# Performance work log

Measured on AMD Instinct MI355X. Metric: run time of the kernel, lower is better.

The kernel has to match this reference:

```python
import jax, jax.numpy as jnp
import numpy as np

N_NODES = 100000
N_EDGES = 1600000
D_IN = 64
D_HID = 64
D_OUT = 64
TOPK = 32


def _num_params(din, dout):
    return din * dout + dout


def setup_inputs() -> dict:
    key = jax.random.key(0)
    ks = jax.random.split(key, 16)
    x = jax.random.normal(ks[0], (N_NODES, D_IN), dtype=jnp.float32)
    edge_index = jax.random.randint(ks[1], (2, N_EDGES), 0, N_NODES, dtype=jnp.int64)
    # GCN layer params (PyG GCNConv: lin.weight [out,in], bias [out])
    w0 = jax.random.normal(ks[2], (D_HID, D_IN), dtype=jnp.float32) * (1.0 / np.sqrt(D_IN))
    b0 = jnp.zeros((D_HID,), dtype=jnp.float32)
    w1 = jax.random.normal(ks[3], (D_OUT, D_HID), dtype=jnp.float32) * (1.0 / np.sqrt(D_HID))
    b1 = jnp.zeros((D_OUT,), dtype=jnp.float32)
    # summarization vectors p (torch.randn init)
    p0 = jax.random.normal(ks[4], (D_IN,), dtype=jnp.float32)
    p1 = jax.random.normal(ks[5], (D_HID,), dtype=jnp.float32)
    # GRU cells: hidden = num_params, input = topk * feature_dim
    np0 = _num_params(D_IN, D_HID)
    np1 = _num_params(D_HID, D_OUT)
    gi0 = TOPK * D_IN
    gi1 = TOPK * D_HID
    s0 = 1.0 / np.sqrt(np0)
    s1 = 1.0 / np.sqrt(np1)
    wih0 = jax.random.uniform(ks[6], (3 * np0, gi0), jnp.float32, -s0, s0)
    whh0 = jax.random.uniform(ks[7], (3 * np0, np0), jnp.float32, -s0, s0)
    bih0 = jax.random.uniform(ks[8], (3 * np0,), jnp.float32, -s0, s0)
    bhh0 = jax.random.uniform(ks[9], (3 * np0,), jnp.float32, -s0, s0)
    wih1 = jax.random.uniform(ks[10], (3 * np1, gi1), jnp.float32, -s1, s1)
    whh1 = jax.random.uniform(ks[11], (3 * np1, np1), jnp.float32, -s1, s1)
    bih1 = jax.random.uniform(ks[12], (3 * np1,), jnp.float32, -s1, s1)
    bhh1 = jax.random.uniform(ks[13], (3 * np1,), jnp.float32, -s1, s1)
    return {"x": x, "edge_index": edge_index,
            "p0": p0, "p1": p1,
            "w0": w0, "b0": b0, "w1": w1, "b1": b1,
            "wih0": wih0, "whh0": whh0, "bih0": bih0, "bhh0": bhh0,
            "wih1": wih1, "whh1": whh1, "bih1": bih1, "bhh1": bhh1}


def _summarize(h, p, k):
    # attention summary: top-k nodes by h @ p_norm, weighted by tanh(score)
    p_norm = p / (jnp.linalg.norm(p) + 1e-8)
    y = h @ p_norm                      # [N]
    _, idx = jax.lax.top_k(y, k)        # k <= N here, matches torch.topk branch
    w = jnp.tanh(y)
    return h[idx] * w[idx][:, None]     # [k, feat]


def _gru_cell(xv, hv, wih, whh, bih, bhh):
    gi = xv @ wih.T + bih
    gh = hv @ whh.T + bhh
    ir, iz, inew = jnp.split(gi, 3)
    hr, hz, hnew = jnp.split(gh, 3)
    r = jax.nn.sigmoid(ir + hr)
    z = jax.nn.sigmoid(iz + hz)
    n = jnp.tanh(inew + r * hnew)
    return (1.0 - z) * n + z * hv


def _gcn_conv(h, src, dst, weight, bias, n_nodes):
    # PyG GCNConv: x' = x @ W.T; add self-loops; sym-norm aggregation; + bias
    xw = h @ weight.T
    loop = jnp.arange(n_nodes, dtype=src.dtype)
    s = jnp.concatenate([src, loop])
    d = jnp.concatenate([dst, loop])
    deg = jax.ops.segment_sum(jnp.ones(s.shape[0], dtype=xw.dtype), d,
                              num_segments=n_nodes)
    dinv = jnp.where(deg > 0, jax.lax.rsqrt(jnp.maximum(deg, 1e-12)), 0.0)
    norm = dinv[s] * dinv[d]
    msgs = xw[s] * norm[:, None]
    out = jax.ops.segment_sum(msgs, d, num_segments=n_nodes)
    return out + bias


def reference(x, edge_index, p0, p1, w0, b0, w1, b1,
              wih0, whh0, bih0, bhh0, wih1, whh1, bih1, bhh1):
    src, dst = edge_index[0], edge_index[1]
    n = x.shape[0]
    h = x
    layers = [
        (p0, w0, b0, wih0, whh0, bih0, bhh0, D_IN, D_HID, True),
        (p1, w1, b1, wih1, whh1, bih1, bhh1, D_HID, D_OUT, False),
    ]
    for (p, w, b, wih, whh, bih, bhh, din, dout, relu) in layers:
        # summarize node embeddings -> GRU input (Z_t.T.flatten(): feature-major)
        Z = _summarize(h, p, TOPK)                  # [TOPK, din]
        z_flat = Z.T.reshape(-1)                    # [din*TOPK]
        # initial GRU hidden = flattened current GCN params (weight then bias)
        h0 = jnp.concatenate([w.reshape(-1), b])    # [din*dout + dout]
        new_w = _gru_cell(z_flat, h0, wih, whh, bih, bhh)
        weight = new_w[: din * dout].reshape(dout, din)
        bias = new_w[din * dout:]
        h = _gcn_conv(h, src, dst, weight, bias, n)
        if relu:
            h = jax.nn.relu(h)  # dropout is identity in eval mode
    return h
```

## Files before the change

kernel.cpp:

```cpp
#include <hip/hip_runtime.h>
#include <math.h>

#define N_NODES 100000
#define N_EDGES 1600000
#define D 64
#define NP 4160
#define GI3 12480
#define GIN 2048
#define TOPK 32

#define NB 391
#define SCAT_ITEMS 4096
#define SCAT_BLKS 391
#define COLCAP 6144

#define OFF_PN     0u
#define OFF_MISC   64u
#define OFF_IDX    80u
#define OFF_WSEL   112u
#define OFF_ZFLAT  144u
#define OFF_NEWW   2192u
#define OFF_GI     6400u
#define OFF_GH     18880u
#define OFF_HIST   31360u
#define OFF_Y      96896u
#define OFF_DEG    196896u
#define OFF_DINV   296896u
#define OFF_ROWPTR 396896u
#define OFF_CURSOR 496898u
#define OFF_COL    596898u
#define OFF_CAND   2196898u
#define OFF_XW     2396898u
#define OFF_H1     8796898u
#define OFF_BSUM   15196898u
#define WS_FLOATS  15197026u

__device__ __forceinline__ unsigned fkey(float f) {
    unsigned u = __float_as_uint(f);
    return u ^ ((u & 0x80000000u) ? 0xFFFFFFFFu : 0x80000000u);
}

__global__ void k_zero32(unsigned* __restrict__ p, int n) {
    int i = blockIdx.x * blockDim.x + threadIdx.x;
    if (i < n) p[i] = 0u;
}

__global__ void k_bcount(const int* __restrict__ dst, unsigned* __restrict__ bcnt, int ne) {
    __shared__ unsigned h[NB];
    int t = threadIdx.x;
    for (int i = t; i < NB; i += 256) h[i] = 0u;
    __syncthreads();
    int base0 = blockIdx.x * SCAT_ITEMS;
    #pragma unroll
    for (int k = 0; k < 16; ++k) {
        int i = base0 + k * 256 + t;
        if (i < ne) atomicAdd(&h[dst[i] >> 8], 1u);
    }
    __syncthreads();
    for (int i = t; i < NB; i += 256) if (h[i]) atomicAdd(&bcnt[i], h[i]);
}

__global__ void k_bscan(const unsigned* __restrict__ bcnt, unsigned* __restrict__ bbase,
                        unsigned* __restrict__ bcur, unsigned* __restrict__ rowptr) {
    __shared__ unsigned sc[512];
    int t = threadIdx.x;
    unsigned v = (t < NB) ? bcnt[t] : 0u;
    sc[t] = v; __syncthreads();
    for (int off = 1; off < 512; off <<= 1) {
        unsigned a = (t >= off) ? sc[t - off] : 0u;
        __syncthreads();
        sc[t] += a;
        __syncthreads();
    }
    unsigned ex = sc[t] - v;
    if (t <= NB) bbase[t] = ex;
    if (t < NB) bcur[t] = ex;
    if (t == 511) rowptr[N_NODES] = sc[511];
}

__global__ void k_bscatter(const int* __restrict__ src, const int* __restrict__ dst,
                           unsigned* __restrict__ bcur, unsigned* __restrict__ ebuf, int ne) {
    __shared__ unsigned hist[NB];
    __shared__ unsigned sc[512];
    __shared__ unsigned basel[NB];
    __shared__ unsigned lcur[NB];
    __shared__ unsigned gdst[NB];
    __shared__ unsigned sbuf[SCAT_ITEMS];
    __shared__ unsigned short sb[SCAT_ITEMS];
    int t = threadIdx.x;
    for (int i = t; i < NB; i += 256) hist[i] = 0u;
    __syncthreads();
    int base0 = blockIdx.x * SCAT_ITEMS;
    unsigned key[16]; int bk[16];
    #pragma unroll
    for (int k = 0; k < 16; ++k) {
        int i = base0 + k * 256 + t;
        if (i < ne) {
            int d = dst[i];
            bk[k] = d >> 8;
            key[k] = ((unsigned)(d & 255) << 24) | (unsigned)src[i];
            atomicAdd(&hist[bk[k]], 1u);
        } else bk[k] = -1;
    }
    __syncthreads();
    {
        unsigned v0 = hist[t];
        unsigned v1 = (t + 256 < NB) ? hist[t + 256] : 0u;
        sc[t] = v0; sc[t + 256] = v1; __syncthreads();
        for (int off = 1; off < 512; off <<= 1) {
            unsigned a0 = (t >= off) ? sc[t - off] : 0u;
            unsigned a1 = (t + 256 >= off) ? sc[t + 256 - off] : 0u;
            __syncthreads();
            sc[t] += a0; sc[t + 256] += a1;
            __syncthreads();
        }
    }
    for (int i = t; i < NB; i += 256) {
        unsigned b0 = sc[i] - hist[i];
        basel[i] = b0; lcur[i] = b0;
    }
    __syncthreads();
    for (int i = t; i < NB; i += 256) if (hist[i]) gdst[i] = atomicAdd(&bcur[i], hist[i]);
    #pragma unroll
    for (int k = 0; k < 16; ++k) if (bk[k] >= 0) {
        unsigned p = atomicAdd(&lcur[bk[k]], 1u);
        sbuf[p] = key[k]; sb[p] = (unsigned short)bk[k];
    }
    __syncthreads();
    int cnt = min(SCAT_ITEMS, ne - base0);
    for (int j = t; j < cnt; j += 256) {
        unsigned b = sb[j];
        ebuf[gdst[b] + ((unsigned)j - basel[b])] = sbuf[j];
    }
}

__global__ void k_bcsr(const unsigned* __restrict__ ebuf, const unsigned* __restrict__ bbase,
                       unsigned* __restrict__ rowptr, float* __restrict__ dinv,
                       int* __restrict__ col, int n) {
    __shared__ unsigned deg[256];
    __shared__ unsigned sc[256];
    __shared__ unsigned lcur[256];
    __shared__ int colbuf[COLCAP];
    int b = blockIdx.x, t = threadIdx.x;
    int lo = b << 8;
    unsigned e0 = bbase[b], e1 = bbase[b + 1];
    deg[t] = 0u; __syncthreads();
    for (unsigned j = e0 + t; j < e1; j += 256) atomicAdd(&deg[ebuf[j] >> 24], 1u);
    __syncthreads();
    sc[t] = deg[t]; __syncthreads();
    for (int off = 1; off < 256; off <<= 1) {
        unsigned a = (t >= off) ? sc[t - off] : 0u;
        __syncthreads();
        sc[t] += a;
        __syncthreads();
    }
    unsigned lrp = sc[t] - deg[t];
    if (lo + t < n) {
        rowptr[lo + t] = e0 + lrp;
        dinv[lo + t] = rsqrtf((float)(deg[t] + 1u));
    }
    lcur[t] = lrp; __syncthreads();
    for (unsigned j = e0 + t; j < e1; j += 256) {
        unsigned k = ebuf[j];
        unsigned p = atomicAdd(&lcur[k >> 24], 1u);
        if (p < COLCAP) colbuf[p] = (int)(k & 0xFFFFFFu);
        else col[e0 + p] = (int)(k & 0xFFFFFFu);
    }
    __syncthreads();
    unsigned cnt = e1 - e0;
    for (unsigned j = t; j < cnt && j < COLCAP; j += 256) col[e0 + j] = colbuf[j];
}

__global__ void k_pnorm(const float* __restrict__ p, float* __restrict__ pn,
                        unsigned* __restrict__ misc) {
    int t = threadIdx.x;
    float v = p[t];
    float s = v * v;
    for (int o = 32; o; o >>= 1) s += __shfl_down(s, o, 64);
    s = __shfl(s, 0, 64);
    pn[t] = v / (sqrtf(s) + 1e-8f);
    if (t < 16) misc[t] = 0u;
}

__global__ void k_y_hist(const float* __restrict__ h, const float* __restrict__ pn,
                         float* __restrict__ y, unsigned* __restrict__ hist, int n) {
    int wave = (blockIdx.x * blockDim.x + threadIdx.x) >> 6;
    int lane = threadIdx.x & 63;
    int nw = (gridDim.x * blockDim.x) >> 6;
    float p = pn[lane];
    for (int i = wave; i < n; i += nw) {
        float v = h[(size_t)i * D + lane] * p;
        for (int o = 32; o; o >>= 1) v += __shfl_down(v, o, 64);
        if (lane == 0) {
            y[i] = v;
            atomicAdd(&hist[fkey(v) >> 16], 1u);
        }
    }
}

__global__ void k_thresh(const unsigned* __restrict__ hist, unsigned* __restrict__ misc) {
    __shared__ unsigned cs[256];
    __shared__ unsigned s2[256];
    __shared__ int tstar;
    int t = threadIdx.x;
    unsigned sum = 0;
    for (int j = 0; j < 256; ++j) sum += hist[t * 256 + j];
    cs[t] = sum; __syncthreads();
    for (int off = 1; off < 256; off <<= 1) {
        unsigned add = (t + off < 256) ? cs[t + off] : 0u;
        __syncthreads();
        cs[t] += add;
        __syncthreads();
    }
    if (cs[t] >= TOPK && (t == 255 || cs[t + 1] < TOPK)) tstar = t;
    __syncthreads();
    int ts = tstar;
    unsigned above = (ts == 255) ? 0u : cs[ts + 1];
    s2[t] = hist[ts * 256 + t]; __syncthreads();
    for (int off = 1; off < 256; off <<= 1) {
        unsigned add = (t + off < 256) ? s2[t + off] : 0u;
        __syncthreads();
        s2[t] += add;
        __syncthreads();
    }
    if (above + s2[t] >= TOPK && (t == 255 || above + s2[t + 1] < TOPK))
        misc[1] = (unsigned)(ts * 256 + t);
}

__global__ void k_compact(const float* __restrict__ y, unsigned* __restrict__ misc,
                          unsigned long long* __restrict__ cand, int n) {
    int i = blockIdx.x * blockDim.x + threadIdx.x;
    if (i >= n) return;
    unsigned thr = misc[1];
    unsigned k = fkey(y[i]);
    if ((k >> 16) >= thr) {
        unsigned pos = atomicAdd(&misc[0], 1u);
        cand[pos] = ((unsigned long long)k << 32) | (unsigned)(0xFFFFFFFFu - (unsigned)i);
    }
}

__global__ void k_select(const float* __restrict__ y, const unsigned* __restrict__ misc,
                         unsigned long long* __restrict__ cand,
                         int* __restrict__ idxb, float* __restrict__ wsel) {
    int t = threadIdx.x;
    int C = (int)misc[0];
    for (int k = 0; k < TOPK; ++k) {
        unsigned long long m = 0ull;
        for (int j = t; j < C; j += 64) { unsigned long long c = cand[j]; if (c > m) m = c; }
        for (int o = 32; o; o >>= 1) {
            unsigned long long other = __shfl_down(m, o, 64);
            if (other > m) m = other;
        }
        unsigned long long best = __shfl(m, 0, 64);
        for (int j = t; j < C; j += 64) if (cand[j] == best) cand[j] = 0ull;
        if (t == 0) {
            int idx = (int)(0xFFFFFFFFu - (unsigned)(best & 0xFFFFFFFFull));
            idxb[k] = idx;
            wsel[k] = tanhf(y[idx]);
        }
    }
}

__global__ void k_zflat(const float* __restrict__ h, const int* __restrict__ idxb,
                        const float* __restrict__ wsel, float* __restrict__ z) {
    int t = blockIdx.x * blockDim.x + threadIdx.x;
    if (t < GIN) {
        int k = t & 31, d = t >> 5;
        z[t] = h[(size_t)idxb[k] * D + d] * wsel[k];
    }
}

__global__ void k_mv(const float* __restrict__ W, const float* __restrict__ bias,
                     const float* __restrict__ vecA, int lenA, const float* __restrict__ vecB,
                     float* __restrict__ out, int rows, int cols) {
    extern __shared__ float v[];
    for (int j = threadIdx.x; j < cols; j += blockDim.x)
        v[j] = (j < lenA) ? vecA[j] : vecB[j - lenA];
    __syncthreads();
    int wave = (blockIdx.x * blockDim.x + threadIdx.x) >> 6;
    int lane = threadIdx.x & 63;
    if (wave >= rows) return;
    const float4* Wr = (const float4*)(W + (size_t)wave * cols);
    int n4 = cols >> 2;
    float acc = 0.f;
    for (int j = lane; j < n4; j += 64) {
        float4 w4 = Wr[j];
        acc += w4.x * v[4 * j] + w4.y * v[4 * j + 1] + w4.z * v[4 * j + 2] + w4.w * v[4 * j + 3];
    }
    for (int o = 32; o; o >>= 1) acc += __shfl_down(acc, o, 64);
    if (lane == 0) out[wave] = acc + bias[wave];
}

__global__ void k_gru(const float* __restrict__ gi, const float* __restrict__ gh,
                      const float* __restrict__ w, const float* __restrict__ b,
                      float* __restrict__ neww) {
    int j = blockIdx.x * blockDim.x + threadIdx.x;
    if (j >= NP) return;
    float r = 1.f / (1.f + expf(-(gi[j] + gh[j])));
    float z = 1.f / (1.f + expf(-(gi[NP + j] + gh[NP + j])));
    float n = tanhf(gi[2 * NP + j] + r * gh[2 * NP + j]);
    float h0 = (j < 4096) ? w[j] : b[j - 4096];
    neww[j] = (1.f - z) * n + z * h0;
}

__global__ void k_xw(const float* __restrict__ h, const float* __restrict__ neww,
                     float* __restrict__ xw, int n) {
    __shared__ float WT[64 * 64];
    for (int t = threadIdx.x; t < 4096; t += blockDim.x) {
        int o = t >> 6, d = t & 63;
        WT[d * 64 + o] = neww[t];
    }
    __syncthreads();
    int wave = (blockIdx.x * blockDim.x + threadIdx.x) >> 6;
    int lane = threadIdx.x & 63;
    int nw = (gridDim.x * blockDim.x) >> 6;
    for (int i = wave; i < n; i += nw) {
        float hv = h[(size_t)i * D + lane];
        float acc = 0.f;
        #pragma unroll 16
        for (int d = 0; d < 64; ++d) {
            float hd = __shfl(hv, d, 64);
            acc += hd * WT[d * 64 + lane];
        }
        xw[(size_t)i * D + lane] = acc;
    }
}

__global__ void k_agg(const float* __restrict__ xw, const float* __restrict__ dinv,
                      const unsigned* __restrict__ rowptr, const int* __restrict__ col,
                      const float* __restrict__ neww, float* __restrict__ out,
                      int n, int relu) {
    int wave = (blockIdx.x * blockDim.x + threadIdx.x) >> 6;
    int lane = threadIdx.x & 63;
    int nw = (gridDim.x * blockDim.x) >> 6;
    float bias = neww[4096 + lane];
    for (int v = wave; v < n; v += nw) {
        unsigned p0 = rowptr[v], p1 = rowptr[v + 1];
        float dv = dinv[v];
        float acc = dv * xw[(size_t)v * D + lane];
        for (unsigned base = p0; base < p1; base += 64) {
            int cnt = (int)min(64u, p1 - base);
            int s = 0; float ds = 0.f;
            if (lane < cnt) { s = col[base + lane]; ds = dinv[s]; }
            for (int j = 0; j < cnt; ++j) {
                int sj = __shfl(s, j, 64);
                float dsj = __shfl(ds, j, 64);
                acc += dsj * xw[(size_t)sj * D + lane];
            }
        }
        float r = bias + dv * acc;
        if (relu) r = fmaxf(r, 0.f);
        out[(size_t)v * D + lane] = r;
    }
}

extern "C" void kernel_launch(void* const* d_in, const int* in_sizes, int n_in,
                              void* d_out, int out_size, void* d_ws, size_t ws_size,
                              hipStream_t stream) {
    if (ws_size < (size_t)WS_FLOATS * 4) return;

    const float* x = (const float*)d_in[0];
    const int* src = (const int*)d_in[1];
    const int* dst = src + N_EDGES;
    const float* P[2]   = {(const float*)d_in[2],  (const float*)d_in[3]};
    const float* W[2]   = {(const float*)d_in[4],  (const float*)d_in[6]};
    const float* B[2]   = {(const float*)d_in[5],  (const float*)d_in[7]};
    const float* WIH[2] = {(const float*)d_in[8],  (const float*)d_in[12]};
    const float* WHH[2] = {(const float*)d_in[9],  (const float*)d_in[13]};
    const float* BIH[2] = {(const float*)d_in[10], (const float*)d_in[14]};
    const float* BHH[2] = {(const float*)d_in[11], (const float*)d_in[15]};

    float* ws = (float*)d_ws;
    float* pn = ws + OFF_PN;
    unsigned* misc = (unsigned*)(ws + OFF_MISC);
    int* idxb = (int*)(ws + OFF_IDX);
    float* wsel = ws + OFF_WSEL;
    float* zflat = ws + OFF_ZFLAT;
    float* neww = ws + OFF_NEWW;
    float* gi = ws + OFF_GI;
    float* gh = ws + OFF_GH;
    unsigned* hist = (unsigned*)(ws + OFF_HIST);
    float* y = ws + OFF_Y;
    unsigned* bcnt  = (unsigned*)(ws + OFF_DEG);
    unsigned* bbase = (unsigned*)(ws + OFF_DEG) + 512;
    unsigned* bcur  = (unsigned*)(ws + OFF_DEG) + 1024;
    float* dinv = ws + OFF_DINV;
    unsigned* rowptr = (unsigned*)(ws + OFF_ROWPTR);
    int* col = (int*)(ws + OFF_COL);
    unsigned long long* cand = (unsigned long long*)(ws + OFF_CAND);
    float* xw = ws + OFF_XW;
    unsigned* ebuf = (unsigned*)(ws + OFF_XW);
    float* h1 = ws + OFF_H1;
    float* out = (float*)d_out;

    hipLaunchKernelGGL(k_zero32, dim3((NB + 255) / 256), dim3(256), 0, stream, bcnt, NB);
    hipLaunchKernelGGL(k_bcount, dim3(SCAT_BLKS), dim3(256), 0, stream, dst, bcnt, N_EDGES);
    hipLaunchKernelGGL(k_bscan, dim3(1), dim3(512), 0, stream, bcnt, bbase, bcur, rowptr);
    hipLaunchKernelGGL(k_bscatter, dim3(SCAT_BLKS), dim3(256), 0, stream, src, dst, bcur, ebuf, N_EDGES);
    hipLaunchKernelGGL(k_bcsr, dim3(NB), dim3(256), 0, stream, ebuf, bbase, rowptr, dinv, col, N_NODES);

    for (int l = 0; l < 2; ++l) {
        const float* h = (l == 0) ? x : h1;
        float* ho = (l == 0) ? h1 : out;
        hipLaunchKernelGGL(k_zero32, dim3(256), dim3(256), 0, stream, hist, 65536);
        hipLaunchKernelGGL(k_pnorm, dim3(1), dim3(64), 0, stream, P[l], pn, misc);
        hipLaunchKernelGGL(k_y_hist, dim3(1024), dim3(256), 0, stream, h, pn, y, hist, N_NODES);
        hipLaunchKernelGGL(k_thresh, dim3(1), dim3(256), 0, stream, hist, misc);
        hipLaunchKernelGGL(k_compact, dim3((N_NODES + 255) / 256), dim3(256), 0, stream, y, misc, cand, N_NODES);
        hipLaunchKernelGGL(k_select, dim3(1), dim3(64), 0, stream, y, misc, cand, idxb, wsel);
        hipLaunchKernelGGL(k_zflat, dim3(8), dim3(256), 0, stream, h, idxb, wsel, zflat);
        hipLaunchKernelGGL(k_mv, dim3(GI3 / 4), dim3(256), GIN * 4, stream,
                           WIH[l], BIH[l], zflat, GIN, zflat, gi, GI3, GIN);
        hipLaunchKernelGGL(k_mv, dim3(GI3 / 4), dim3(256), NP * 4, stream,
                           WHH[l], BHH[l], W[l], 4096, B[l], gh, GI3, NP);
        hipLaunchKernelGGL(k_gru, dim3((NP + 255) / 256), dim3(256), 0, stream, gi, gh, W[l], B[l], neww);
        hipLaunchKernelGGL(k_xw, dim3(2048), dim3(256), 0, stream, h, neww, xw, N_NODES);
        hipLaunchKernelGGL(k_agg, dim3(4096), dim3(256), 0, stream, xw, dinv, rowptr, col, neww, ho,
                           N_NODES, (l == 0) ? 1 : 0);
    }
}
```

Baseline: 1.378 ms.

## Fuse launches, prescale xw by dinv, unroll y-hist reduction

Merges histogram zeroing into the p-normalisation kernel and runs the two GRU matrix-vector products in a single launch. The source degree normalisation is folded into the xw write, so aggregation no longer gathers dinv per edge or shuffles it. The y/histogram kernel now processes four rows per wave iteration to overlap loads and reductions. The aggregation gather is the main cost, and each edge in it now needs one fewer dependent load.

```diff
diff --git a/kernel.cpp b/kernel.cpp
--- a/kernel.cpp
+++ b/kernel.cpp
@@ -8,6 +8,7 @@
 #define GI3 12480
 #define GIN 2048
 #define TOPK 32
+#define MV_BLKS 3120
 
 #define NB 391
 #define SCAT_ITEMS 4096
@@ -171,15 +172,21 @@
     for (unsigned j = t; j < cnt && j < COLCAP; j += 256) col[e0 + j] = colbuf[j];
 }
 
-__global__ void k_pnorm(const float* __restrict__ p, float* __restrict__ pn,
-                        unsigned* __restrict__ misc) {
-    int t = threadIdx.x;
-    float v = p[t];
-    float s = v * v;
-    for (int o = 32; o; o >>= 1) s += __shfl_down(s, o, 64);
-    s = __shfl(s, 0, 64);
-    pn[t] = v / (sqrtf(s) + 1e-8f);
-    if (t < 16) misc[t] = 0u;
+__global__ void k_pnorm_zh(const float* __restrict__ p, float* __restrict__ pn,
+                           unsigned* __restrict__ misc, unsigned* __restrict__ hist) {
+    int g = blockIdx.x * blockDim.x + threadIdx.x;
+    hist[g] = 0u;
+    if (blockIdx.x == 0) {
+        int t = threadIdx.x;
+        if (t < 64) {
+            float v = p[t];
+            float s = v * v;
+            for (int o = 32; o; o >>= 1) s += __shfl_down(s, o, 64);
+            s = __shfl(s, 0, 64);
+            pn[t] = v / (sqrtf(s) + 1e-8f);
+        }
+        if (t < 16) misc[t] = 0u;
+    }
 }
 
 __global__ void k_y_hist(const float* __restrict__ h, const float* __restrict__ pn,
@@ -188,12 +195,24 @@
     int lane = threadIdx.x & 63;
     int nw = (gridDim.x * blockDim.x) >> 6;
     float p = pn[lane];
-    for (int i = wave; i < n; i += nw) {
-        float v = h[(size_t)i * D + lane] * p;
-        for (int o = 32; o; o >>= 1) v += __shfl_down(v, o, 64);
+    for (int i = wave; i < n; i += 4 * nw) {
+        int i1 = i + nw, i2 = i + 2 * nw, i3 = i + 3 * nw;
+        float v0 = h[(size_t)i * D + lane] * p;
+        float v1 = (i1 < n) ? h[(size_t)i1 * D + lane] * p : 0.f;
+        float v2 = (i2 < n) ? h[(size_t)i2 * D + lane] * p : 0.f;
+        float v3 = (i3 < n) ? h[(size_t)i3 * D + lane] * p : 0.f;
+        #pragma unroll
+        for (int o = 32; o; o >>= 1) {
+            v0 += __shfl_down(v0, o, 64);
+            v1 += __shfl_down(v1, o, 64);
+            v2 += __shfl_down(v2, o, 64);
+            v3 += __shfl_down(v3, o, 64);
+        }
         if (lane == 0) {
-            y[i] = v;
-            atomicAdd(&hist[fkey(v) >> 16], 1u);
+            y[i] = v0; atomicAdd(&hist[fkey(v0) >> 16], 1u);
+            if (i1 < n) { y[i1] = v1; atomicAdd(&hist[fkey(v1) >> 16], 1u); }
+            if (i2 < n) { y[i2] = v2; atomicAdd(&hist[fkey(v2) >> 16], 1u); }
+            if (i3 < n) { y[i3] = v3; atomicAdd(&hist[fkey(v3) >> 16], 1u); }
         }
     }
 }
@@ -270,17 +289,29 @@
     }
 }
 
-__global__ void k_mv(const float* __restrict__ W, const float* __restrict__ bias,
-                     const float* __restrict__ vecA, int lenA, const float* __restrict__ vecB,
-                     float* __restrict__ out, int rows, int cols) {
+__global__ void k_mv2(const float* __restrict__ W0, const float* __restrict__ bia0,
+                      const float* __restrict__ vA0, int lenA0, const float* __restrict__ vB0,
+                      float* __restrict__ out0, int cols0,
+                      const float* __restrict__ W1, const float* __restrict__ bia1,
+                      const float* __restrict__ vA1, int lenA1, const float* __restrict__ vB1,
+                      float* __restrict__ out1, int cols1) {
     extern __shared__ float v[];
+    int seg = (blockIdx.x >= MV_BLKS);
+    const float* W    = seg ? W1   : W0;
+    const float* bias = seg ? bia1 : bia0;
+    const float* vA   = seg ? vA1  : vA0;
+    const float* vB   = seg ? vB1  : vB0;
+    float* out        = seg ? out1 : out0;
+    int lenA          = seg ? lenA1 : lenA0;
+    int cols          = seg ? cols1 : cols0;
+    int lb = blockIdx.x - (seg ? MV_BLKS : 0);
     for (int j = threadIdx.x; j < cols; j += blockDim.x)
-        v[j] = (j < lenA) ? vecA[j] : vecB[j - lenA];
-    __syncthreads();
-    int wave = (blockIdx.x * blockDim.x + threadIdx.x) >> 6;
+        v[j] = (j < lenA) ? vA[j] : vB[j - lenA];
+    __syncthreads();
+    int row = ((lb * blockDim.x + threadIdx.x) >> 6);
     int lane = threadIdx.x & 63;
-    if (wave >= rows) return;
-    const float4* Wr = (const float4*)(W + (size_t)wave * cols);
+    if (row >= GI3) return;
+    const float4* Wr = (const float4*)(W + (size_t)row * cols);
     int n4 = cols >> 2;
     float acc = 0.f;
     for (int j = lane; j < n4; j += 64) {
@@ -288,7 +319,7 @@
         acc += w4.x * v[4 * j] + w4.y * v[4 * j + 1] + w4.z * v[4 * j + 2] + w4.w * v[4 * j + 3];
     }
     for (int o = 32; o; o >>= 1) acc += __shfl_down(acc, o, 64);
-    if (lane == 0) out[wave] = acc + bias[wave];
+    if (lane == 0) out[row] = acc + bias[row];
 }
 
 __global__ void k_gru(const float* __restrict__ gi, const float* __restrict__ gh,
@@ -304,7 +335,7 @@
 }
 
 __global__ void k_xw(const float* __restrict__ h, const float* __restrict__ neww,
-                     float* __restrict__ xw, int n) {
+                     const float* __restrict__ dinv, float* __restrict__ sxw, int n) {
     __shared__ float WT[64 * 64];
     for (int t = threadIdx.x; t < 4096; t += blockDim.x) {
         int o = t >> 6, d = t & 63;
@@ -322,11 +353,11 @@
             float hd = __shfl(hv, d, 64);
             acc += hd * WT[d * 64 + lane];
         }
-        xw[(size_t)i * D + lane] = acc;
-    }
-}
-
-__global__ void k_agg(const float* __restrict__ xw, const float* __restrict__ dinv,
+        sxw[(size_t)i * D + lane] = dinv[i] * acc;
+    }
+}
+
+__global__ void k_agg(const float* __restrict__ sxw, const float* __restrict__ dinv,
                       const unsigned* __restrict__ rowptr, const int* __restrict__ col,
                       const float* __restrict__ neww, float* __restrict__ out,
                       int n, int relu) {
@@ -337,15 +368,14 @@
     for (int v = wave; v < n; v += nw) {
         unsigned p0 = rowptr[v], p1 = rowptr[v + 1];
         float dv = dinv[v];
-        float acc = dv * xw[(size_t)v * D + lane];
+        float acc = sxw[(size_t)v * D + lane];
         for (unsigned base = p0; base < p1; base += 64) {
             int cnt = (int)min(64u, p1 - base);
-            int s = 0; float ds = 0.f;
-            if (lane < cnt) { s = col[base + lane]; ds = dinv[s]; }
+            int s = 0;
+            if (lane < cnt) s = col[base + lane];
             for (int j = 0; j < cnt; ++j) {
                 int sj = __shfl(s, j, 64);
-                float dsj = __shfl(ds, j, 64);
-                acc += dsj * xw[(size_t)sj * D + lane];
+                acc += sxw[(size_t)sj * D + lane];
             }
         }
         float r = bias + dv * acc;
@@ -402,19 +432,17 @@
     for (int l = 0; l < 2; ++l) {
         const float* h = (l == 0) ? x : h1;
         float* ho = (l == 0) ? h1 : out;
-        hipLaunchKernelGGL(k_zero32, dim3(256), dim3(256), 0, stream, hist, 65536);
-        hipLaunchKernelGGL(k_pnorm, dim3(1), dim3(64), 0, stream, P[l], pn, misc);
+        hipLaunchKernelGGL(k_pnorm_zh, dim3(256), dim3(256), 0, stream, P[l], pn, misc, hist);
         hipLaunchKernelGGL(k_y_hist, dim3(1024), dim3(256), 0, stream, h, pn, y, hist, N_NODES);
         hipLaunchKernelGGL(k_thresh, dim3(1), dim3(256), 0, stream, hist, misc);
         hipLaunchKernelGGL(k_compact, dim3((N_NODES + 255) / 256), dim3(256), 0, stream, y, misc, cand, N_NODES);
         hipLaunchKernelGGL(k_select, dim3(1), dim3(64), 0, stream, y, misc, cand, idxb, wsel);
         hipLaunchKernelGGL(k_zflat, dim3(8), dim3(256), 0, stream, h, idxb, wsel, zflat);
-        hipLaunchKernelGGL(k_mv, dim3(GI3 / 4), dim3(256), GIN * 4, stream,
-                           WIH[l], BIH[l], zflat, GIN, zflat, gi, GI3, GIN);
-        hipLaunchKernelGGL(k_mv, dim3(GI3 / 4), dim3(256), NP * 4, stream,
-                           WHH[l], BHH[l], W[l], 4096, B[l], gh, GI3, NP);
+        hipLaunchKernelGGL(k_mv2, dim3(2 * MV_BLKS), dim3(256), NP * 4, stream,
+                           WIH[l], BIH[l], zflat, GIN, zflat, gi, GIN,
+                           WHH[l], BHH[l], W[l], 4096, B[l], gh, NP);
         hipLaunchKernelGGL(k_gru, dim3((NP + 255) / 256), dim3(256), 0, stream, gi, gh, W[l], B[l], neww);
-        hipLaunchKernelGGL(k_xw, dim3(2048), dim3(256), 0, stream, h, neww, xw, N_NODES);
+        hipLaunchKernelGGL(k_xw, dim3(2048), dim3(256), 0, stream, h, neww, dinv, xw, N_NODES);
         hipLaunchKernelGGL(k_agg, dim3(4096), dim3(256), 0, stream, xw, dinv, rowptr, col, neww, ho,
                            N_NODES, (l == 0) ? 1 : 0);
     }
```

Result: no change. 1.362 ms (-1.2%).
